# Optimization experiments

Measured on AMD Instinct MI355X. Metric: run time of the kernel, lower is better.

The kernel has to match this reference:

```python
import jax, jax.numpy as jnp
import numpy as np

NUM_HEADS = 8


def _rel_to_abs(x):
    # x: [b, h, l, 2l-1] relative logits -> [b, h, l, l] absolute logits
    b, h, l, _ = x.shape
    x = jnp.pad(x, ((0, 0), (0, 0), (0, 0), (0, 1)))          # [b,h,l,2l]
    x = x.reshape(b, h, l * 2 * l)
    x = jnp.pad(x, ((0, 0), (0, 0), (0, l - 1)))               # [b,h,2l^2+l-1]
    x = x.reshape(b, h, l + 1, 2 * l - 1)
    return x[:, :, :l, l - 1:]                                 # [b,h,l,l]


def setup_inputs() -> dict:
    key = jax.random.key(0)
    k1, k2, k3 = jax.random.split(key, 3)
    B, H, D, L = 8, NUM_HEADS, 64, 512
    std = D ** (-0.5)
    qkv = jax.random.normal(k1, (B, 3 * H * D, L), dtype=jnp.float32)
    k_emb = jax.random.normal(k2, (H, 2 * L - 1, D), dtype=jnp.float32) * std
    v_emb = jax.random.normal(k3, (H, 2 * L - 1, D), dtype=jnp.float32) * std
    return {"qkv": qkv, "k_emb": k_emb, "v_emb": v_emb}


def reference(qkv, k_emb, v_emb):
    # qkv: [B, 3*H*D, L]; k_emb/v_emb: [H, 2L-1, D]
    B, C3, L = qkv.shape
    H = NUM_HEADS
    D = C3 // (3 * H)
    x = qkv.reshape(B, H, 3 * D, L)
    q = jnp.transpose(x[:, :, :D, :], (0, 1, 3, 2))          # [B,H,L,D]
    k = jnp.transpose(x[:, :, D:2 * D, :], (0, 1, 3, 2))
    v = jnpp = jnp.transpose(x[:, :, 2 * D:, :], (0, 1, 3, 2))
    logits = jnp.einsum('bhld,bhmd->bhlm', q, k)             # [B,H,L,L] (no 1/sqrt(d) scale in original)
    rel_logits = jnp.einsum('bhld,hmd->bhlm', q, k_emb)      # [B,H,L,2L-1]
    logits = logits + _rel_to_abs(rel_logits)
    weights = jax.nn.softmax(logits, axis=-1)
    out = jnp.einsum('bhlm,bhmd->bhld', weights, v)          # [B,H,L,D]
    # add_relative_to_values=False in module, so v_emb is unused (parameter only)
    return out.reshape(B, -1, L)                              # [B, H*D, L] via raw reshape, as in torch
```

## Files before the change

### kernel.cpp

```cpp
#include <hip/hip_runtime.h>
#include <hip/hip_bf16.h>

#define NH 8
#define DH 64
#define SL 512

typedef __bf16 bf16x8 __attribute__((ext_vector_type(8)));
typedef float f32x16 __attribute__((ext_vector_type(16)));
typedef float f32x4 __attribute__((ext_vector_type(4)));
typedef unsigned int u32;

#define MFMA(a, b, c) __builtin_amdgcn_mfma_f32_32x32x16_bf16(a, b, c, 0, 0, 0)
#define ZERO16 {0.f,0.f,0.f,0.f,0.f,0.f,0.f,0.f,0.f,0.f,0.f,0.f,0.f,0.f,0.f,0.f}

union BF8 { unsigned short s[8]; bf16x8 v; };

__device__ __forceinline__ unsigned short f2bf(float x) {
    union { float f; u32 u; } v; v.f = x;
    return (unsigned short)((v.u + 0x7fffu + ((v.u >> 16) & 1u)) >> 16);
}
__device__ __forceinline__ float bf2f(unsigned short s) {
    union { u32 u; float f; } v; v.u = ((u32)s) << 16; return v.f;
}
__device__ __forceinline__ void loadsplit8(const float* p, bf16x8& h8, bf16x8& l8) {
    f32x4 a = *(const f32x4*)p;
    f32x4 b = *(const f32x4*)(p + 4);
    BF8 uh, ul;
#pragma unroll
    for (int i = 0; i < 4; ++i) {
        unsigned short h0 = f2bf(a[i]); uh.s[i]     = h0; ul.s[i]     = f2bf(a[i] - bf2f(h0));
        unsigned short h1 = f2bf(b[i]); uh.s[4 + i] = h1; ul.s[4 + i] = f2bf(b[i] - bf2f(h1));
    }
    h8 = uh.v; l8 = ul.v;
}

__global__ void detect_dtype_kernel(const unsigned short* __restrict__ q, int* __restrict__ flag) {
    int t = threadIdx.x;
    unsigned int u = (unsigned int)q[t];
    float f = __uint_as_float(u << 16);
    bool big = !(fabsf(f) <= 1e4f);
    unsigned long long vote = __ballot(big);
    __shared__ int any;
    if (t == 0) any = 0;
    __syncthreads();
    if (vote != 0ull && (t & 63) == 0) atomicOr(&any, 1);
    __syncthreads();
    if (t == 0) *flag = any;
}

__device__ __forceinline__ float ldv(const __hip_bfloat16* p) { return __bfloat162float(*p); }
__device__ __forceinline__ float ldv(const float* p) { return *p; }
__device__ __forceinline__ void stv(__hip_bfloat16* p, float v) { *p = __float2bfloat16(v); }
__device__ __forceinline__ void stv(float* p, float v) { *p = v; }

__global__ __launch_bounds__(256, 2) void attn_flash_f32(
    const float* __restrict__ qkv,
    const float* __restrict__ k_emb,
    float* __restrict__ out,
    const int* __restrict__ flag)
{
    if (*flag != 1) return;
    const int bid = blockIdx.x;
    const int swz = (bid & 7) * 64 + (bid >> 3);
    const int bh = swz >> 3, lt = swz & 7;
    const int h  = bh & (NH - 1);
    const int t = threadIdx.x;
    const int wid = t >> 6, lane = t & 63;
    const int lo = lane & 31, hi = lane >> 5;
    const int slab = wid & 1, mh = wid >> 1;
    const int l0w = lt * 64 + slab * 32;

    __shared__ __align__(16) unsigned char smem[51712];
    unsigned short (*skh)[32][72] = (unsigned short (*)[32][72])(smem);
    unsigned short (*skl)[32][72] = (unsigned short (*)[32][72])(smem + 9216);
    float* rect = (float*)(smem + 18432) + wid * 2048;
    unsigned short (*sqh)[72] = (unsigned short (*)[72])(smem + 18432);
    unsigned short (*sql)[72] = (unsigned short (*)[72])(smem + 18432 + 9216);
    float* sstat = (float*)(smem + 18432 + 32768);

    const float* qbase = qkv + (size_t)bh * (3 * DH * SL);
    const float* kglob = qbase + DH * SL;
    const float* vflat = qbase + (size_t)2 * DH * SL;
    const float* ebase = k_emb + (size_t)h * (2 * SL - 1) * DH;

    {
        const int d = t >> 2, c = (t & 3) * 16;
        const float* src = qbase + (size_t)d * SL + lt * 64 + c;
#pragma unroll
        for (int g = 0; g < 4; ++g) {
            f32x4 x = *(const f32x4*)(src + 4 * g);
#pragma unroll
            for (int i = 0; i < 4; ++i) {
                unsigned short hb = f2bf(x[i]);
                sqh[c + 4 * g + i][d] = hb;
                sql[c + 4 * g + i][d] = f2bf(x[i] - bf2f(hb));
            }
        }
    }
    {
        const int tid2 = slab * 64 + lane;
        const int d = tid2 >> 1, mo = (tid2 & 1) << 4;
        const float* src = kglob + (size_t)d * SL + mh * 256 + mo;
#pragma unroll
        for (int g = 0; g < 4; ++g) {
            f32x4 x = *(const f32x4*)(src + 4 * g);
#pragma unroll
            for (int i = 0; i < 4; ++i) {
                unsigned short hb = f2bf(x[i]);
                skh[mh][mo + 4 * g + i][d] = hb;
                skl[mh][mo + 4 * g + i][d] = f2bf(x[i] - bf2f(hb));
            }
        }
    }
    __syncthreads();

    bf16x8 qfh[4], qfl[4];
#pragma unroll
    for (int ds = 0; ds < 4; ++ds) {
        qfh[ds] = *(const bf16x8*)&sqh[slab * 32 + lo][16 * ds + 8 * hi];
        qfl[ds] = *(const bf16x8*)&sql[slab * 32 + lo][16 * ds + 8 * hi];
    }
    __syncthreads();

    const int sw = (lo & 7) << 2;
    float* rrow = rect + lo * 64;

    f32x16 o0 = ZERO16, o1 = ZERO16;
    float mx = -1e30f, sum = 0.f;

    for (int step = 0; step < 8; ++step) {
        const int m0 = mh * 256 + step * 32;
        const int rb = m0 - l0w + 480;

        int r1 = rb + 32 + lo; if (r1 > 1022) r1 = 1022;
        const float* e0p = ebase + (size_t)(rb + lo) * DH;
        const float* e1p = ebase + (size_t)r1 * DH;
        bf16x8 ea[4], ec[4];
#pragma unroll
        for (int ds = 0; ds < 4; ++ds) {
            const int off = 16 * ds + 8 * hi;
            f32x4 a0 = *(const f32x4*)(e0p + off);
            f32x4 a1 = *(const f32x4*)(e0p + off + 4);
            f32x4 c0 = *(const f32x4*)(e1p + off);
            f32x4 c1 = *(const f32x4*)(e1p + off + 4);
            BF8 ua, uc;
#pragma unroll
            for (int i = 0; i < 4; ++i) {
                ua.s[i] = f2bf(a0[i]); ua.s[4 + i] = f2bf(a1[i]);
                uc.s[i] = f2bf(c0[i]); uc.s[4 + i] = f2bf(c1[i]);
            }
            ea[ds] = ua.v; ec[ds] = uc.v;
        }
        const float* v0p = vflat + (size_t)lo * SL + m0 + 8 * hi;
        const float* v1p = vflat + (size_t)(32 + lo) * SL + m0 + 8 * hi;
        bf16x8 v00h, v00l, v01h, v01l, v10h, v10l, v11h, v11l;
        loadsplit8(v0p,      v00h, v00l);
        loadsplit8(v0p + 16, v01h, v01l);
        loadsplit8(v1p,      v10h, v10l);
        loadsplit8(v1p + 16, v11h, v11l);

        f32x16 ra = ZERO16, rc = ZERO16, sacc = ZERO16;
#pragma unroll
        for (int ds = 0; ds < 4; ++ds) {
            bf16x8 kh = *(const bf16x8*)&skh[mh][lo][16 * ds + 8 * hi];
            bf16x8 kl = *(const bf16x8*)&skl[mh][lo][16 * ds + 8 * hi];
            sacc = MFMA(kh, qfh[ds], sacc);
            sacc = MFMA(kh, qfl[ds], sacc);
            sacc = MFMA(kl, qfh[ds], sacc);
            ra   = MFMA(ea[ds], qfh[ds], ra);
            rc   = MFMA(ec[ds], qfh[ds], rc);
        }

#pragma unroll
        for (int g = 0; g < 4; ++g) {
            const int j0 = 8 * g + 4 * hi;
            f32x4 w0 = { ra[4 * g], ra[4 * g + 1], ra[4 * g + 2], ra[4 * g + 3] };
            f32x4 w1 = { rc[4 * g], rc[4 * g + 1], rc[4 * g + 2], rc[4 * g + 3] };
            *(f32x4*)(rrow + (j0 ^ sw))        = w0;
            *(f32x4*)(rrow + ((j0 + 32) ^ sw)) = w1;
        }
        float s[16];
#pragma unroll
        for (int r = 0; r < 16; ++r) {
            const int mp = (r & 3) + 8 * (r >> 2) + 4 * hi;
            s[r] = sacc[r] + rrow[(mp + 31 - lo) ^ sw];
        }

        float tmx = s[0];
#pragma unroll
        for (int r = 1; r < 16; ++r) tmx = fmaxf(tmx, s[r]);
        tmx = fmaxf(tmx, __shfl_xor(tmx, 32, 64));
        const float nmx = fmaxf(mx, tmx);
        if (__any(nmx > mx)) {
            const float sc = __expf(mx - nmx);
#pragma unroll
            for (int r = 0; r < 16; ++r) { o0[r] *= sc; o1[r] *= sc; }
            sum *= sc;
            mx = nmx;
        }
        u32 pk[8], xk[8];
        float ps = 0.f;
#pragma unroll
        for (int q2 = 0; q2 < 8; ++q2) {
            union { __hip_bfloat162 b; u32 u; } cv;
            cv.b = __float22bfloat162_rn(make_float2(__expf(s[2 * q2] - mx),
                                                     __expf(s[2 * q2 + 1] - mx)));
            pk[q2] = cv.u;
            float2 g2 = __bfloat1622float2(cv.b);
            ps += g2.x + g2.y;
        }
        sum += ps;
#pragma unroll
        for (int q2 = 0; q2 < 8; ++q2) xk[q2] = (u32)__shfl_xor((int)pk[q2], 32, 64);

        union { u32 u[4]; bf16x8 v; } pf0, pf1;
        if (hi == 0) {
            pf0.u[0] = pk[0]; pf0.u[1] = pk[1]; pf0.u[2] = xk[0]; pf0.u[3] = xk[1];
            pf1.u[0] = pk[4]; pf1.u[1] = pk[5]; pf1.u[2] = xk[4]; pf1.u[3] = xk[5];
        } else {
            pf0.u[0] = xk[2]; pf0.u[1] = xk[3]; pf0.u[2] = pk[2]; pf0.u[3] = pk[3];
            pf1.u[0] = xk[6]; pf1.u[1] = xk[7]; pf1.u[2] = pk[6]; pf1.u[3] = pk[7];
        }
        o0 = MFMA(v00h, pf0.v, o0);
        o0 = MFMA(v00l, pf0.v, o0);
        o0 = MFMA(v01h, pf1.v, o0);
        o0 = MFMA(v01l, pf1.v, o0);
        o1 = MFMA(v10h, pf0.v, o1);
        o1 = MFMA(v10l, pf0.v, o1);
        o1 = MFMA(v11h, pf1.v, o1);
        o1 = MFMA(v11l, pf1.v, o1);

        if (step < 7) {
            __syncthreads();
            const int m0n = mh * 256 + (step + 1) * 32;
            const int tid2 = slab * 64 + lane;
            const int d = tid2 >> 1, mo = (tid2 & 1) << 4;
            const float* src = kglob + (size_t)d * SL + m0n + mo;
#pragma unroll
            for (int g = 0; g < 4; ++g) {
                f32x4 x = *(const f32x4*)(src + 4 * g);
#pragma unroll
                for (int i = 0; i < 4; ++i) {
                    unsigned short hb = f2bf(x[i]);
                    skh[mh][mo + 4 * g + i][d] = hb;
                    skl[mh][mo + 4 * g + i][d] = f2bf(x[i] - bf2f(hb));
                }
            }
            __syncthreads();
        }
    }

    sum += __shfl_xor(sum, 32, 64);

    if (mh == 1) {
        if (hi == 0) { sstat[slab * 64 + lo] = mx; sstat[slab * 64 + 32 + lo] = sum; }
        float* ob = rect;
#pragma unroll
        for (int r = 0; r < 16; ++r) {
            const int d0 = (r & 3) + 8 * (r >> 2) + 4 * hi;
            ob[d0 * 32 + lo]        = o0[r];
            ob[(32 + d0) * 32 + lo] = o1[r];
        }
    }
    __syncthreads();
    if (mh == 0) {
        const float mx1 = sstat[slab * 64 + lo], s1 = sstat[slab * 64 + 32 + lo];
        const float nm = fmaxf(mx, mx1);
        const float a0 = __expf(mx - nm);
        const float a1 = __expf(mx1 - nm);
        const float inv = 1.f / (a0 * sum + a1 * s1);
        const float* ob = (float*)(smem + 18432) + (wid + 2) * 2048;
        float* orow = out + ((size_t)bh * SL + l0w + lo) * DH;
#pragma unroll
        for (int r = 0; r < 16; r += 2) {
            const int d0 = (r & 3) + 8 * (r >> 2) + 4 * hi;
            float2 w0 = make_float2((a0 * o0[r]     + a1 * ob[d0 * 32 + lo]) * inv,
                                    (a0 * o0[r + 1] + a1 * ob[(d0 + 1) * 32 + lo]) * inv);
            *(float2*)(orow + d0) = w0;
            float2 w1 = make_float2((a0 * o1[r]     + a1 * ob[(32 + d0) * 32 + lo]) * inv,
                                    (a0 * o1[r + 1] + a1 * ob[(32 + d0 + 1) * 32 + lo]) * inv);
            *(float2*)(orow + 32 + d0) = w1;
        }
    }
}

template <typename T, int MODE>
__global__ __launch_bounds__(256) void attn_rel_kernel(
    const T* __restrict__ qkv, const T* __restrict__ k_emb,
    T* __restrict__ out, const int* __restrict__ flag)
{
    if (*flag != MODE) return;
    const int t = threadIdx.x;
    __shared__ float s_q[DH];
    __shared__ float s_w[SL];
    __shared__ float s_red[24];
    __shared__ float s_part[256];

    for (int it = 0; it < 16; ++it) {
        const int bid = blockIdx.x * 16 + it;
        const int l   = bid & (SL - 1);
        const int bh  = bid >> 9;
        const int h   = bh & (NH - 1);
        const long base = (long)bh * (3 * DH) * SL;

        __syncthreads();
        if (t < DH) s_q[t] = ldv(&qkv[base + (long)t * SL + l]);
        __syncthreads();

        const T* kp = qkv + base + (long)DH * SL;
        const T* ke = k_emb + (long)h * (2 * SL - 1) * DH;
        float lg[2];
#pragma unroll
        for (int i = 0; i < 2; ++i) {
            const int m = t + i * 256;
            float acc = 0.f;
#pragma unroll 8
            for (int d = 0; d < DH; ++d)
                acc += s_q[d] * ldv(&kp[(long)d * SL + m]);
            const int r = m - l + (SL - 1);
            const T* kr = ke + (long)r * DH;
            float acc2 = 0.f;
#pragma unroll 8
            for (int d = 0; d < DH; ++d)
                acc2 += s_q[d] * ldv(&kr[d]);
            lg[i] = acc + acc2;
        }

        float mxv = fmaxf(lg[0], lg[1]);
        for (int off = 32; off > 0; off >>= 1)
            mxv = fmaxf(mxv, __shfl_down(mxv, off, 64));
        if ((t & 63) == 0) s_red[t >> 6] = mxv;
        __syncthreads();
        if (t == 0)
            s_red[8] = fmaxf(fmaxf(s_red[0], s_red[1]), fmaxf(s_red[2], s_red[3]));
        __syncthreads();
        mxv = s_red[8];

        const float e0 = expf(lg[0] - mxv);
        const float e1 = expf(lg[1] - mxv);
        s_w[t] = e0;
        s_w[t + 256] = e1;
        float sm = e0 + e1;
        for (int off = 32; off > 0; off >>= 1)
            sm += __shfl_down(sm, off, 64);
        if ((t & 63) == 0) s_red[16 + (t >> 6)] = sm;
        __syncthreads();
        const float inv = 1.0f / (s_red[16] + s_red[17] + s_red[18] + s_red[19]);

        const T* vp = qkv + base + (long)(2 * DH) * SL;
        const int g  = t >> 6;
        const int dd = t & 63;
        const T* vrow = vp + (long)dd * SL + g * 128;
        const float* wrow = s_w + g * 128;
        float acc = 0.f;
#pragma unroll 8
        for (int m = 0; m < 128; ++m)
            acc += wrow[m] * ldv(&vrow[m]);
        s_part[t] = acc;
        __syncthreads();
        if (t < 64) {
            float o = (s_part[t] + s_part[t + 64] + s_part[t + 128] + s_part[t + 192]) * inv;
            stv(&out[((long)bh * SL + l) * DH + t], o);
        }
    }
}

extern "C" void kernel_launch(void* const* d_in, const int* in_sizes, int n_in,
                              void* d_out, int out_size, void* d_ws, size_t ws_size,
                              hipStream_t stream) {
    (void)in_sizes; (void)n_in; (void)out_size; (void)ws_size;
    int* flag = (int*)d_ws;

    detect_dtype_kernel<<<1, 256, 0, stream>>>((const unsigned short*)d_in[0], flag);

    attn_flash_f32<<<512, 256, 0, stream>>>(
        (const float*)d_in[0], (const float*)d_in[1], (float*)d_out, flag);

    attn_rel_kernel<__hip_bfloat16, 0><<<2048, 256, 0, stream>>>(
        (const __hip_bfloat16*)d_in[0], (const __hip_bfloat16*)d_in[1],
        (__hip_bfloat16*)d_out, flag);
}
```

Baseline: 128.0 us.

## Split KV range across four waves per 32-query tile, drop LDS K staging

Each block now handles 32 query rows, with its four waves each covering a 128-key quarter, and the grid doubles to 1024 blocks. K is loaded and split into bf16 hi/lo directly from global memory into registers, replacing the LDS staging and per-step block barriers. The relative-embedding fragment is carried over from one step to the next so only one new embedding tile is converted per step. s_setprio is placed around the MFMA bursts, launch bounds target 3 blocks per CU, and a four-way softmax merge replaces the two-way one. The trade-off is strided uncoalesced global loads for Q and K and more register pressure.

Result: slower. 207.4 us (+62.0%).

```diff
diff --git a/kernel.cpp b/kernel.cpp
--- a/kernel.cpp
+++ b/kernel.cpp
@@ -13,25 +13,28 @@
 #define MFMA(a, b, c) __builtin_amdgcn_mfma_f32_32x32x16_bf16(a, b, c, 0, 0, 0)
 #define ZERO16 {0.f,0.f,0.f,0.f,0.f,0.f,0.f,0.f,0.f,0.f,0.f,0.f,0.f,0.f,0.f,0.f}
 
-union BF8 { unsigned short s[8]; bf16x8 v; };
-
 __device__ __forceinline__ unsigned short f2bf(float x) {
     union { float f; u32 u; } v; v.f = x;
     return (unsigned short)((v.u + 0x7fffu + ((v.u >> 16) & 1u)) >> 16);
 }
-__device__ __forceinline__ float bf2f(unsigned short s) {
-    union { u32 u; float f; } v; v.u = ((u32)s) << 16; return v.f;
-}
-__device__ __forceinline__ void loadsplit8(const float* p, bf16x8& h8, bf16x8& l8) {
-    f32x4 a = *(const f32x4*)p;
-    f32x4 b = *(const f32x4*)(p + 4);
-    BF8 uh, ul;
+
+__device__ __forceinline__ void split8(const f32x4 a, const f32x4 b, bf16x8& h8, bf16x8& l8) {
+    union { __hip_bfloat16 s[8]; bf16x8 v; } uh, ul;
 #pragma unroll
     for (int i = 0; i < 4; ++i) {
-        unsigned short h0 = f2bf(a[i]); uh.s[i]     = h0; ul.s[i]     = f2bf(a[i] - bf2f(h0));
-        unsigned short h1 = f2bf(b[i]); uh.s[4 + i] = h1; ul.s[4 + i] = f2bf(b[i] - bf2f(h1));
+        __hip_bfloat16 h0 = __float2bfloat16(a[i]);
+        __hip_bfloat16 h1 = __float2bfloat16(b[i]);
+        uh.s[i] = h0; uh.s[4 + i] = h1;
+        ul.s[i]     = __float2bfloat16(a[i] - __bfloat162float(h0));
+        ul.s[4 + i] = __float2bfloat16(b[i] - __bfloat162float(h1));
     }
     h8 = uh.v; l8 = ul.v;
+}
+__device__ __forceinline__ void cvt8(const f32x4 a, const f32x4 b, bf16x8& h8) {
+    union { unsigned short s[8]; bf16x8 v; } uh;
+#pragma unroll
+    for (int i = 0; i < 4; ++i) { uh.s[i] = f2bf(a[i]); uh.s[4 + i] = f2bf(b[i]); }
+    h8 = uh.v;
 }
 
 __global__ void detect_dtype_kernel(const unsigned short* __restrict__ q, int* __restrict__ flag) {
@@ -53,7 +56,7 @@
 __device__ __forceinline__ void stv(__hip_bfloat16* p, float v) { *p = __float2bfloat16(v); }
 __device__ __forceinline__ void stv(float* p, float v) { *p = v; }
 
-__global__ __launch_bounds__(256, 2) void attn_flash_f32(
+__global__ __launch_bounds__(256, 3) void attn_flash_f32(
     const float* __restrict__ qkv,
     const float* __restrict__ k_emb,
     float* __restrict__ out,
@@ -61,115 +64,93 @@
 {
     if (*flag != 1) return;
     const int bid = blockIdx.x;
-    const int swz = (bid & 7) * 64 + (bid >> 3);
-    const int bh = swz >> 3, lt = swz & 7;
+    const int swz = (bid & 7) * 128 + (bid >> 3);
+    const int bh = swz >> 4, lt = swz & 15;
     const int h  = bh & (NH - 1);
     const int t = threadIdx.x;
     const int wid = t >> 6, lane = t & 63;
     const int lo = lane & 31, hi = lane >> 5;
-    const int slab = wid & 1, mh = wid >> 1;
-    const int l0w = lt * 64 + slab * 32;
-
-    __shared__ __align__(16) unsigned char smem[51712];
-    unsigned short (*skh)[32][72] = (unsigned short (*)[32][72])(smem);
-    unsigned short (*skl)[32][72] = (unsigned short (*)[32][72])(smem + 9216);
-    float* rect = (float*)(smem + 18432) + wid * 2048;
-    unsigned short (*sqh)[72] = (unsigned short (*)[72])(smem + 18432);
-    unsigned short (*sql)[72] = (unsigned short (*)[72])(smem + 18432 + 9216);
-    float* sstat = (float*)(smem + 18432 + 32768);
+    const int mq = wid;
+    const int l0 = lt * 32;
+
+    __shared__ float srect[4][2048];
+    __shared__ float sstat[4][2][32];
 
     const float* qbase = qkv + (size_t)bh * (3 * DH * SL);
     const float* kglob = qbase + DH * SL;
     const float* vflat = qbase + (size_t)2 * DH * SL;
     const float* ebase = k_emb + (size_t)h * (2 * SL - 1) * DH;
 
+    bf16x8 qfh[4], qfl[4];
+#pragma unroll
+    for (int ds = 0; ds < 4; ++ds) {
+        const float* qp = qbase + (size_t)(16 * ds + 8 * hi) * SL + (l0 + lo);
+        f32x4 xa, xb;
+#pragma unroll
+        for (int i = 0; i < 4; ++i) { xa[i] = qp[(size_t)i * SL]; xb[i] = qp[(size_t)(4 + i) * SL]; }
+        split8(xa, xb, qfh[ds], qfl[ds]);
+    }
+
+    const int rb0 = mq * 128 - l0 + 480;
+    bf16x8 eah[4];
     {
-        const int d = t >> 2, c = (t & 3) * 16;
-        const float* src = qbase + (size_t)d * SL + lt * 64 + c;
-#pragma unroll
-        for (int g = 0; g < 4; ++g) {
-            f32x4 x = *(const f32x4*)(src + 4 * g);
-#pragma unroll
-            for (int i = 0; i < 4; ++i) {
-                unsigned short hb = f2bf(x[i]);
-                sqh[c + 4 * g + i][d] = hb;
-                sql[c + 4 * g + i][d] = f2bf(x[i] - bf2f(hb));
-            }
-        }
-    }
-    {
-        const int tid2 = slab * 64 + lane;
-        const int d = tid2 >> 1, mo = (tid2 & 1) << 4;
-        const float* src = kglob + (size_t)d * SL + mh * 256 + mo;
-#pragma unroll
-        for (int g = 0; g < 4; ++g) {
-            f32x4 x = *(const f32x4*)(src + 4 * g);
-#pragma unroll
-            for (int i = 0; i < 4; ++i) {
-                unsigned short hb = f2bf(x[i]);
-                skh[mh][mo + 4 * g + i][d] = hb;
-                skl[mh][mo + 4 * g + i][d] = f2bf(x[i] - bf2f(hb));
-            }
-        }
-    }
-    __syncthreads();
-
-    bf16x8 qfh[4], qfl[4];
-#pragma unroll
-    for (int ds = 0; ds < 4; ++ds) {
-        qfh[ds] = *(const bf16x8*)&sqh[slab * 32 + lo][16 * ds + 8 * hi];
-        qfl[ds] = *(const bf16x8*)&sql[slab * 32 + lo][16 * ds + 8 * hi];
-    }
-    __syncthreads();
-
+        const float* e0p = ebase + (size_t)(rb0 + lo) * DH;
+#pragma unroll
+        for (int ds = 0; ds < 4; ++ds) {
+            const int off = 16 * ds + 8 * hi;
+            cvt8(*(const f32x4*)(e0p + off), *(const f32x4*)(e0p + off + 4), eah[ds]);
+        }
+    }
+
+    float* rect = srect[wid];
+    float* rrow = rect + lo * 64;
     const int sw = (lo & 7) << 2;
-    float* rrow = rect + lo * 64;
 
     f32x16 o0 = ZERO16, o1 = ZERO16;
     float mx = -1e30f, sum = 0.f;
 
-    for (int step = 0; step < 8; ++step) {
-        const int m0 = mh * 256 + step * 32;
-        const int rb = m0 - l0w + 480;
-
-        int r1 = rb + 32 + lo; if (r1 > 1022) r1 = 1022;
-        const float* e0p = ebase + (size_t)(rb + lo) * DH;
-        const float* e1p = ebase + (size_t)r1 * DH;
-        bf16x8 ea[4], ec[4];
+    for (int step = 0; step < 4; ++step) {
+        const int m0 = mq * 128 + step * 32;
+        const int rb = rb0 + step * 32;
+
+        bf16x8 kh[4], kl[4];
 #pragma unroll
         for (int ds = 0; ds < 4; ++ds) {
-            const int off = 16 * ds + 8 * hi;
-            f32x4 a0 = *(const f32x4*)(e0p + off);
-            f32x4 a1 = *(const f32x4*)(e0p + off + 4);
-            f32x4 c0 = *(const f32x4*)(e1p + off);
-            f32x4 c1 = *(const f32x4*)(e1p + off + 4);
-            BF8 ua, uc;
-#pragma unroll
-            for (int i = 0; i < 4; ++i) {
-                ua.s[i] = f2bf(a0[i]); ua.s[4 + i] = f2bf(a1[i]);
-                uc.s[i] = f2bf(c0[i]); uc.s[4 + i] = f2bf(c1[i]);
+            const float* kp = kglob + (size_t)(16 * ds + 8 * hi) * SL + (m0 + lo);
+            f32x4 xa, xb;
+#pragma unroll
+            for (int i = 0; i < 4; ++i) { xa[i] = kp[(size_t)i * SL]; xb[i] = kp[(size_t)(4 + i) * SL]; }
+            split8(xa, xb, kh[ds], kl[ds]);
+        }
+        bf16x8 ech[4];
+        {
+            int r1 = rb + 32 + lo; if (r1 > 1022) r1 = 1022;
+            const float* e1p = ebase + (size_t)r1 * DH;
+#pragma unroll
+            for (int ds = 0; ds < 4; ++ds) {
+                const int off = 16 * ds + 8 * hi;
+                cvt8(*(const f32x4*)(e1p + off), *(const f32x4*)(e1p + off + 4), ech[ds]);
             }
-            ea[ds] = ua.v; ec[ds] = uc.v;
         }
         const float* v0p = vflat + (size_t)lo * SL + m0 + 8 * hi;
         const float* v1p = vflat + (size_t)(32 + lo) * SL + m0 + 8 * hi;
         bf16x8 v00h, v00l, v01h, v01l, v10h, v10l, v11h, v11l;
-        loadsplit8(v0p,      v00h, v00l);
-        loadsplit8(v0p + 16, v01h, v01l);
-        loadsplit8(v1p,      v10h, v10l);
-        loadsplit8(v1p + 16, v11h, v11l);
+        split8(*(const f32x4*)v0p,        *(const f32x4*)(v0p + 4),  v00h, v00l);
+        split8(*(const f32x4*)(v0p + 16), *(const f32x4*)(v0p + 20), v01h, v01l);
+        split8(*(const f32x4*)v1p,        *(const f32x4*)(v1p + 4),  v10h, v10l);
+        split8(*(const f32x4*)(v1p + 16), *(const f32x4*)(v1p + 20), v11h, v11l);
 
         f32x16 ra = ZERO16, rc = ZERO16, sacc = ZERO16;
+        __builtin_amdgcn_s_setprio(1);
 #pragma unroll
         for (int ds = 0; ds < 4; ++ds) {
-            bf16x8 kh = *(const bf16x8*)&skh[mh][lo][16 * ds + 8 * hi];
-            bf16x8 kl = *(const bf16x8*)&skl[mh][lo][16 * ds + 8 * hi];
-            sacc = MFMA(kh, qfh[ds], sacc);
-            sacc = MFMA(kh, qfl[ds], sacc);
-            sacc = MFMA(kl, qfh[ds], sacc);
-            ra   = MFMA(ea[ds], qfh[ds], ra);
-            rc   = MFMA(ec[ds], qfh[ds], rc);
-        }
+            sacc = MFMA(kh[ds], qfh[ds], sacc);
+            sacc = MFMA(kh[ds], qfl[ds], sacc);
+            sacc = MFMA(kl[ds], qfh[ds], sacc);
+            ra   = MFMA(eah[ds], qfh[ds], ra);
+            rc   = MFMA(ech[ds], qfh[ds], rc);
+        }
+        __builtin_amdgcn_s_setprio(0);
 
 #pragma unroll
         for (int g = 0; g < 4; ++g) {
@@ -221,6 +202,7 @@
             pf0.u[0] = xk[2]; pf0.u[1] = xk[3]; pf0.u[2] = pk[2]; pf0.u[3] = pk[3];
             pf1.u[0] = xk[6]; pf1.u[1] = xk[7]; pf1.u[2] = pk[6]; pf1.u[3] = pk[7];
         }
+        __builtin_amdgcn_s_setprio(1);
         o0 = MFMA(v00h, pf0.v, o0);
         o0 = MFMA(v00l, pf0.v, o0);
         o0 = MFMA(v01h, pf1.v, o0);
@@ -229,31 +211,16 @@
         o1 = MFMA(v10l, pf0.v, o1);
         o1 = MFMA(v11h, pf1.v, o1);
         o1 = MFMA(v11l, pf1.v, o1);
-
-        if (step < 7) {
-            __syncthreads();
-            const int m0n = mh * 256 + (step + 1) * 32;
-            const int tid2 = slab * 64 + lane;
-            const int d = tid2 >> 1, mo = (tid2 & 1) << 4;
-            const float* src = kglob + (size_t)d * SL + m0n + mo;
-#pragma unroll
-            for (int g = 0; g < 4; ++g) {
-                f32x4 x = *(const f32x4*)(src + 4 * g);
-#pragma unroll
-                for (int i = 0; i < 4; ++i) {
-                    unsigned short hb = f2bf(x[i]);
-                    skh[mh][mo + 4 * g + i][d] = hb;
-                    skl[mh][mo + 4 * g + i][d] = f2bf(x[i] - bf2f(hb));
-                }
-            }
-            __syncthreads();
-        }
+        __builtin_amdgcn_s_setprio(0);
+
+#pragma unroll
+        for (int ds = 0; ds < 4; ++ds) eah[ds] = ech[ds];
     }
 
     sum += __shfl_xor(sum, 32, 64);
 
-    if (mh == 1) {
-        if (hi == 0) { sstat[slab * 64 + lo] = mx; sstat[slab * 64 + 32 + lo] = sum; }
+    if (wid > 0) {
+        if (hi == 0) { sstat[wid][0][lo] = mx; sstat[wid][1][lo] = sum; }
         float* ob = rect;
 #pragma unroll
         for (int r = 0; r < 16; ++r) {
@@ -263,22 +230,30 @@
         }
     }
     __syncthreads();
-    if (mh == 0) {
-        const float mx1 = sstat[slab * 64 + lo], s1 = sstat[slab * 64 + 32 + lo];
-        const float nm = fmaxf(mx, mx1);
+    if (wid == 0) {
+        const float m1 = sstat[1][0][lo], s1 = sstat[1][1][lo];
+        const float m2 = sstat[2][0][lo], s2 = sstat[2][1][lo];
+        const float m3 = sstat[3][0][lo], s3 = sstat[3][1][lo];
+        const float nm = fmaxf(fmaxf(mx, m1), fmaxf(m2, m3));
         const float a0 = __expf(mx - nm);
-        const float a1 = __expf(mx1 - nm);
-        const float inv = 1.f / (a0 * sum + a1 * s1);
-        const float* ob = (float*)(smem + 18432) + (wid + 2) * 2048;
-        float* orow = out + ((size_t)bh * SL + l0w + lo) * DH;
+        const float a1 = __expf(m1 - nm);
+        const float a2 = __expf(m2 - nm);
+        const float a3 = __expf(m3 - nm);
+        const float inv = 1.f / (a0 * sum + a1 * s1 + a2 * s2 + a3 * s3);
+        const float* ob1 = srect[1];
+        const float* ob2 = srect[2];
+        const float* ob3 = srect[3];
+        float* orow = out + ((size_t)bh * SL + l0 + lo) * DH;
 #pragma unroll
         for (int r = 0; r < 16; r += 2) {
             const int d0 = (r & 3) + 8 * (r >> 2) + 4 * hi;
-            float2 w0 = make_float2((a0 * o0[r]     + a1 * ob[d0 * 32 + lo]) * inv,
-                                    (a0 * o0[r + 1] + a1 * ob[(d0 + 1) * 32 + lo]) * inv);
+            float2 w0 = make_float2(
+                (a0 * o0[r]     + a1 * ob1[d0 * 32 + lo] + a2 * ob2[d0 * 32 + lo] + a3 * ob3[d0 * 32 + lo]) * inv,
+                (a0 * o0[r + 1] + a1 * ob1[(d0 + 1) * 32 + lo] + a2 * ob2[(d0 + 1) * 32 + lo] + a3 * ob3[(d0 + 1) * 32 + lo]) * inv);
             *(float2*)(orow + d0) = w0;
-            float2 w1 = make_float2((a0 * o1[r]     + a1 * ob[(32 + d0) * 32 + lo]) * inv,
-                                    (a0 * o1[r + 1] + a1 * ob[(32 + d0 + 1) * 32 + lo]) * inv);
+            float2 w1 = make_float2(
+                (a0 * o1[r]     + a1 * ob1[(32 + d0) * 32 + lo] + a2 * ob2[(32 + d0) * 32 + lo] + a3 * ob3[(32 + d0) * 32 + lo]) * inv,
+                (a0 * o1[r + 1] + a1 * ob1[(32 + d0 + 1) * 32 + lo] + a2 * ob2[(32 + d0 + 1) * 32 + lo] + a3 * ob3[(32 + d0 + 1) * 32 + lo]) * inv);
             *(float2*)(orow + 32 + d0) = w1;
         }
     }
@@ -373,7 +348,7 @@
 
     detect_dtype_kernel<<<1, 256, 0, stream>>>((const unsigned short*)d_in[0], flag);
 
-    attn_flash_f32<<<512, 256, 0, stream>>>(
+    attn_flash_f32<<<1024, 256, 0, stream>>>(
         (const float*)d_in[0], (const float*)d_in[1], (float*)d_out, flag);
 
     attn_rel_kernel<__hip_bfloat16, 0><<<2048, 256, 0, stream>>>(
```
